# Kernel tuning notes

Measured on AMD Instinct MI355X. Metric: run time of the kernel, lower is better.

The kernel has to match this reference:

```python
import jax, jax.numpy as jnp
import numpy as np

OUT_H, OUT_W = 7, 7
SPATIAL_SCALE = 1.0  # aligned=True (align_corners=True interpolate), per init_kwargs


def setup_inputs() -> dict:
    key = jax.random.key(0)
    kf, kb, kx, ky, kw, kh = jax.random.split(key, 6)
    B, C, H, W = 4, 256, 200, 200
    N = 512
    features = jax.random.normal(kf, (B, C, H, W), dtype=jnp.float32)
    batch_idx = jax.random.randint(kb, (N,), 0, B, dtype=jnp.int32)
    # integer boxes with x2>x1, y2>y1, strictly inside the map
    x1 = jax.random.randint(kx, (N,), 0, W - 64, dtype=jnp.int32)
    y1 = jax.random.randint(ky, (N,), 0, H - 64, dtype=jnp.int32)
    bw = jax.random.randint(kw, (N,), 8, 64, dtype=jnp.int32)
    bh = jax.random.randint(kh, (N,), 8, 64, dtype=jnp.int32)
    x2 = jnp.minimum(x1 + bw, W - 1)
    y2 = jnp.minimum(y1 + bh, H - 1)
    rois = jnp.stack([batch_idx, x1, y1, x2, y2], axis=1)  # [N, 5] int32
    return {"features": features, "rois": rois}


def reference(features, rois):
    # features: [B, C, H, W]; rois: [N, 5] int32 (batch, x1, y1, x2, y2)
    # Faithful to: crop features[b, :, y1:y2+1, x1:x2+1] then
    # F.interpolate(size=(7,7), mode='bilinear', align_corners=True).
    N = rois.shape[0]
    H, W = features.shape[2], features.shape[3]
    b = rois[:, 0]
    coords = rois[:, 1:5].astype(jnp.float32) * SPATIAL_SCALE
    x1, y1, x2, y2 = coords[:, 0], coords[:, 1], coords[:, 2], coords[:, 3]

    # align_corners=True source coords inside the crop, offset into the full map
    jy = jnp.arange(OUT_H, dtype=jnp.float32)
    jx = jnp.arange(OUT_W, dtype=jnp.float32)
    sy = y1[:, None] + jy[None, :] * (y2 - y1)[:, None] / (OUT_H - 1)  # [N, OH]
    sx = x1[:, None] + jx[None, :] * (x2 - x1)[:, None] / (OUT_W - 1)  # [N, OW]

    y0f = jnp.floor(sy); x0f = jnp.floor(sx)
    wy = sy - y0f                                  # [N, OH]
    wx = sx - x0f                                  # [N, OW]
    y0 = jnp.clip(y0f.astype(jnp.int32), 0, H - 1)
    y1i = jnp.clip(y0 + 1, 0, H - 1)
    x0 = jnp.clip(x0f.astype(jnp.int32), 0, W - 1)
    x1i = jnp.clip(x0 + 1, 0, W - 1)

    bb = b[:, None, None]                          # [N,1,1]

    def gather(yi, xi):
        # advanced indexing -> [N, OH, OW, C]
        return features[bb, :, yi[:, :, None], xi[:, None, :]]

    v00 = gather(y0, x0)
    v01 = gather(y0, x1i)
    v10 = gather(y1i, x0)
    v11 = gather(y1i, x1i)

    wyb = wy[:, :, None, None]                     # [N, OH, 1, 1]
    wxb = wx[:, None, :, None]                     # [N, 1, OW, 1]
    out = (v00 * (1 - wyb) * (1 - wxb) + v01 * (1 - wyb) * wxb
           + v10 * wyb * (1 - wxb) + v11 * wyb * wxb)  # [N, OH, OW, C]
    return jnp.transpose(out, (0, 3, 1, 2))        # [N, C, OH, OW]
```

## Files before the change

kernel.cpp:

```cpp
#include <hip/hip_runtime.h>
#include <hip/hip_bf16.h>
#include <string.h>

#define OUT_H 7
#define OUT_W 7
#define FEAT_H 200
#define FEAT_W 200
#define HWB  64
#define LSTR 258

__device__ inline unsigned pack2_bf16(float a, float b) {
    __hip_bfloat16 ha = __float2bfloat16(a);
    __hip_bfloat16 hb = __float2bfloat16(b);
    unsigned short ua, ub;
    memcpy(&ua, &ha, 2);
    memcpy(&ub, &hb, 2);
    return (unsigned)ua | ((unsigned)ub << 16);
}

__global__ __launch_bounds__(256) void nchw_to_nhwc_bf16(
    const float* __restrict__ in,
    __hip_bfloat16* __restrict__ out,
    int HW)
{
    __shared__ float tile[HWB * LSTR];
    int hw0 = blockIdx.x * HWB;
    int b   = blockIdx.y;
    const float* inb = in + (size_t)b * 256 * HW;

    int lane = threadIdx.x & 63;
    int wave = threadIdx.x >> 6;
    int hw   = hw0 + lane;

#pragma unroll 8
    for (int cc = 0; cc < 64; ++cc) {
        int c = (wave << 6) + cc;
        tile[lane * LSTR + c] = inb[(size_t)c * HW + hw];
    }
    __syncthreads();

    unsigned* ob = (unsigned*)(out + ((size_t)b * HW + hw0) * 256);
    int t = threadIdx.x;
#pragma unroll 4
    for (int i = 0; i < 32; ++i) {
        int p   = i * 256 + t;
        int j2  = p * 2;
        int hwr = j2 >> 8;
        int c   = j2 & 255;
        float2 v = *(const float2*)&tile[hwr * LSTR + c];
        ob[p] = pack2_bf16(v.x, v.y);
    }
}

__global__ __launch_bounds__(256) void roialign_nhwc_bf16(
    const __hip_bfloat16* __restrict__ featT,
    const int*   __restrict__ rois,
    float*       __restrict__ out)
{
    __shared__ float acc[256 * OUT_H * OUT_W];
    const int H = FEAT_H, W = FEAT_W;
    int n = blockIdx.x;
    int c = threadIdx.x;

    const int* r = rois + n * 5;
    int   b   = r[0];
    float x1f = (float)r[1];
    float y1f = (float)r[2];
    float dx  = (float)r[3] - x1f;
    float dy  = (float)r[4] - y1f;

    const __hip_bfloat16* fb = featT + (size_t)b * (H * W) * 256 + c;

    for (int jy = 0; jy < OUT_H; ++jy) {
        float sy   = y1f + ((float)jy * dy) / (float)(OUT_H - 1);
        float y0fl = floorf(sy);
        float wy   = sy - y0fl;
        int y0  = min(max((int)y0fl, 0), H - 1);
        int y1i = min(y0 + 1, H - 1);
        float omwy = 1.0f - wy;
        const __hip_bfloat16* row0 = fb + (size_t)(y0  * W) * 256;
        const __hip_bfloat16* row1 = fb + (size_t)(y1i * W) * 256;

#pragma unroll
        for (int jx = 0; jx < OUT_W; ++jx) {
            float sx   = x1f + ((float)jx * dx) / (float)(OUT_W - 1);
            float x0fl = floorf(sx);
            float wx   = sx - x0fl;
            int x0  = min(max((int)x0fl, 0), W - 1);
            int x1i = min(x0 + 1, W - 1);
            float omwx = 1.0f - wx;

            float v00 = __bfloat162float(row0[(size_t)x0  * 256]);
            float v01 = __bfloat162float(row0[(size_t)x1i * 256]);
            float v10 = __bfloat162float(row1[(size_t)x0  * 256]);
            float v11 = __bfloat162float(row1[(size_t)x1i * 256]);

            acc[c * (OUT_H * OUT_W) + jy * OUT_W + jx] =
                v00 * omwy * omwx + v01 * omwy * wx +
                v10 * wy   * omwx + v11 * wy   * wx;
        }
    }
    __syncthreads();

    float* ob = out + (size_t)n * 256 * (OUT_H * OUT_W);
    int total = 256 * OUT_H * OUT_W;
    for (int k = c; k < total; k += blockDim.x)
        ob[k] = acc[k];
}

__global__ __launch_bounds__(256) void roialign_direct(
    const float* __restrict__ feat, const int* __restrict__ rois,
    float* __restrict__ out, int C, int total)
{
    int idx = blockIdx.x * blockDim.x + threadIdx.x;
    if (idx >= total) return;
    const int H = FEAT_H, W = FEAT_W;
    int jx = idx % OUT_W;
    int t  = idx / OUT_W;
    int jy = t % OUT_H;
    t /= OUT_H;
    int c = t % C;
    int n = t / C;
    const int* r = rois + n * 5;
    int b = r[0];
    float x1 = (float)r[1], y1 = (float)r[2];
    float x2 = (float)r[3], y2 = (float)r[4];
    float sy = y1 + ((float)jy * (y2 - y1)) / (float)(OUT_H - 1);
    float sx = x1 + ((float)jx * (x2 - x1)) / (float)(OUT_W - 1);
    float y0f = floorf(sy), x0f = floorf(sx);
    float wy = sy - y0f, wx = sx - x0f;
    int y0  = min(max((int)y0f, 0), H - 1);
    int y1i = min(y0 + 1, H - 1);
    int x0  = min(max((int)x0f, 0), W - 1);
    int x1i = min(x0 + 1, W - 1);
    const float* fp = feat + ((size_t)b * C + c) * (size_t)(H * W);
    float v00 = fp[y0  * W + x0 ];
    float v01 = fp[y0  * W + x1i];
    float v10 = fp[y1i * W + x0 ];
    float v11 = fp[y1i * W + x1i];
    float omwy = 1.0f - wy, omwx = 1.0f - wx;
    out[idx] = v00 * omwy * omwx + v01 * omwy * wx
             + v10 * wy   * omwx + v11 * wy   * wx;
}

extern "C" void kernel_launch(void* const* d_in, const int* in_sizes, int n_in,
                              void* d_out, int out_size, void* d_ws, size_t ws_size,
                              hipStream_t stream)
{
    const float* feat = (const float*)d_in[0];
    const int*   rois = (const int*)d_in[1];
    float*       out  = (float*)d_out;

    int N  = in_sizes[1] / 5;
    int C  = out_size / (N * OUT_H * OUT_W);
    int HW = FEAT_H * FEAT_W;
    int B  = in_sizes[0] / (C * HW);

    size_t need = (size_t)B * HW * C * sizeof(__hip_bfloat16);
    if (C == 256 && (HW % HWB) == 0 && ws_size >= need) {
        __hip_bfloat16* featT = (__hip_bfloat16*)d_ws;
        dim3 tgrid(HW / HWB, B, 1);
        nchw_to_nhwc_bf16<<<tgrid, 256, 0, stream>>>(feat, featT, HW);
        roialign_nhwc_bf16<<<N, 256, 0, stream>>>(featT, rois, out);
    } else {
        int total = out_size;
        roialign_direct<<<(total + 255) / 256, 256, 0, stream>>>(feat, rois, out, C, total);
    }
}
```

Before: 260.8 us.

## Vectorize NHWC bf16 transpose and ROI gather with wider loads

The NCHW-to-NHWC bf16 transpose now reads float4 along HW and writes packed uint2 (four bf16 channels) per thread, using a smaller 32-position tile with a padded stride. The ROI-align kernel has each thread handle four channels via uint2 loads, with four thread groups splitting the 49 output points, and unpacks bf16 with bit shifts. The aim is fewer, wider memory transactions in both the transpose (the dominant full-tensor pass) and the gather. It adds possible LDS bank conflicts from the strided scalar tile writes and the acc stores.

```diff
diff --git a/kernel.cpp b/kernel.cpp
--- a/kernel.cpp
+++ b/kernel.cpp
@@ -6,8 +6,9 @@
 #define OUT_W 7
 #define FEAT_H 200
 #define FEAT_W 200
-#define HWB  64
-#define LSTR 258
+#define HW_ALL (FEAT_H * FEAT_W)
+#define HWB  32
+#define LSTR 260
 
 __device__ inline unsigned pack2_bf16(float a, float b) {
     __hip_bfloat16 ha = __float2bfloat16(a);
@@ -18,50 +19,56 @@
     return (unsigned)ua | ((unsigned)ub << 16);
 }
 
-__global__ __launch_bounds__(256) void nchw_to_nhwc_bf16(
+__global__ __launch_bounds__(256) void nchw_to_nhwc_bf16_v2(
     const float* __restrict__ in,
-    __hip_bfloat16* __restrict__ out,
+    unsigned*    __restrict__ outu,
     int HW)
 {
     __shared__ float tile[HWB * LSTR];
     int hw0 = blockIdx.x * HWB;
     int b   = blockIdx.y;
-    const float* inb = in + (size_t)b * 256 * HW;
+    const float* inb = in + (size_t)b * 256 * HW + hw0;
 
     int lane = threadIdx.x & 63;
-    int wave = threadIdx.x >> 6;
-    int hw   = hw0 + lane;
+    int w    = threadIdx.x >> 6;
+    int cg   = lane >> 3;
+    int xq   = lane & 7;
+    int hwr  = xq << 2;
 
-#pragma unroll 8
-    for (int cc = 0; cc < 64; ++cc) {
-        int c = (wave << 6) + cc;
-        tile[lane * LSTR + c] = inb[(size_t)c * HW + hw];
+#pragma unroll
+    for (int cc = 0; cc < 8; ++cc) {
+        int c = (w << 6) + (cc << 3) + cg;
+        float4 v = *(const float4*)(inb + (size_t)c * HW + hwr);
+        tile[(hwr + 0) * LSTR + c] = v.x;
+        tile[(hwr + 1) * LSTR + c] = v.y;
+        tile[(hwr + 2) * LSTR + c] = v.z;
+        tile[(hwr + 3) * LSTR + c] = v.w;
     }
     __syncthreads();
 
-    unsigned* ob = (unsigned*)(out + ((size_t)b * HW + hw0) * 256);
+    uint2* ob = (uint2*)outu + ((size_t)b * HW + hw0) * 64;
     int t = threadIdx.x;
-#pragma unroll 4
-    for (int i = 0; i < 32; ++i) {
-        int p   = i * 256 + t;
-        int j2  = p * 2;
-        int hwr = j2 >> 8;
-        int c   = j2 & 255;
-        float2 v = *(const float2*)&tile[hwr * LSTR + c];
-        ob[p] = pack2_bf16(v.x, v.y);
+#pragma unroll
+    for (int i = 0; i < 8; ++i) {
+        int q2  = (i << 8) + t;
+        int hr  = q2 >> 6;
+        int c0  = (q2 & 63) << 2;
+        float4 v = *(const float4*)&tile[hr * LSTR + c0];
+        uint2 o;
+        o.x = pack2_bf16(v.x, v.y);
+        o.y = pack2_bf16(v.z, v.w);
+        ob[q2] = o;
     }
 }
 
-__global__ __launch_bounds__(256) void roialign_nhwc_bf16(
-    const __hip_bfloat16* __restrict__ featT,
+__global__ __launch_bounds__(256) void roialign_nhwc_v2(
+    const uint2* __restrict__ featT2,
     const int*   __restrict__ rois,
     float*       __restrict__ out)
 {
     __shared__ float acc[256 * OUT_H * OUT_W];
     const int H = FEAT_H, W = FEAT_W;
     int n = blockIdx.x;
-    int c = threadIdx.x;
-
     const int* r = rois + n * 5;
     int   b   = r[0];
     float x1f = (float)r[1];
@@ -69,42 +76,54 @@
     float dx  = (float)r[3] - x1f;
     float dy  = (float)r[4] - y1f;
 
-    const __hip_bfloat16* fb = featT + (size_t)b * (H * W) * 256 + c;
+    int t  = threadIdx.x;
+    int pg = t >> 6;
+    int cq = t & 63;
+    const uint2* fb = featT2 + (size_t)b * HW_ALL * 64 + cq;
 
-    for (int jy = 0; jy < OUT_H; ++jy) {
-        float sy   = y1f + ((float)jy * dy) / (float)(OUT_H - 1);
-        float y0fl = floorf(sy);
-        float wy   = sy - y0fl;
-        int y0  = min(max((int)y0fl, 0), H - 1);
-        int y1i = min(y0 + 1, H - 1);
-        float omwy = 1.0f - wy;
-        const __hip_bfloat16* row0 = fb + (size_t)(y0  * W) * 256;
-        const __hip_bfloat16* row1 = fb + (size_t)(y1i * W) * 256;
+#define BFLO(u) __uint_as_float((u) << 16)
+#define BFHI(u) __uint_as_float((u) & 0xffff0000u)
 
 #pragma unroll
-        for (int jx = 0; jx < OUT_W; ++jx) {
-            float sx   = x1f + ((float)jx * dx) / (float)(OUT_W - 1);
-            float x0fl = floorf(sx);
-            float wx   = sx - x0fl;
+    for (int pi = 0; pi < 13; ++pi) {
+        int p = (pi << 2) + pg;
+        if (p < 49) {
+            int jy = p / 7, jx = p % 7;
+            float sy = y1f + ((float)jy * dy) / 6.0f;
+            float sx = x1f + ((float)jx * dx) / 6.0f;
+            float y0fl = floorf(sy), x0fl = floorf(sx);
+            float wy = sy - y0fl,    wx = sx - x0fl;
+            int y0  = min(max((int)y0fl, 0), H - 1);
+            int y1i = min(y0 + 1, H - 1);
             int x0  = min(max((int)x0fl, 0), W - 1);
             int x1i = min(x0 + 1, W - 1);
-            float omwx = 1.0f - wx;
+            float omwy = 1.0f - wy, omwx = 1.0f - wx;
+            float w00 = omwy * omwx, w01 = omwy * wx;
+            float w10 = wy * omwx,   w11 = wy * wx;
 
-            float v00 = __bfloat162float(row0[(size_t)x0  * 256]);
-            float v01 = __bfloat162float(row0[(size_t)x1i * 256]);
-            float v10 = __bfloat162float(row1[(size_t)x0  * 256]);
-            float v11 = __bfloat162float(row1[(size_t)x1i * 256]);
+            const uint2* row0 = fb + (size_t)(y0  * W) * 64;
+            const uint2* row1 = fb + (size_t)(y1i * W) * 64;
+            uint2 u00 = row0[(size_t)x0  * 64];
+            uint2 u01 = row0[(size_t)x1i * 64];
+            uint2 u10 = row1[(size_t)x0  * 64];
+            uint2 u11 = row1[(size_t)x1i * 64];
 
-            acc[c * (OUT_H * OUT_W) + jy * OUT_W + jx] =
-                v00 * omwy * omwx + v01 * omwy * wx +
-                v10 * wy   * omwx + v11 * wy   * wx;
+            float r0 = BFLO(u00.x)*w00 + BFLO(u01.x)*w01 + BFLO(u10.x)*w10 + BFLO(u11.x)*w11;
+            float r1 = BFHI(u00.x)*w00 + BFHI(u01.x)*w01 + BFHI(u10.x)*w10 + BFHI(u11.x)*w11;
+            float r2 = BFLO(u00.y)*w00 + BFLO(u01.y)*w01 + BFLO(u10.y)*w10 + BFLO(u11.y)*w11;
+            float r3 = BFHI(u00.y)*w00 + BFHI(u01.y)*w01 + BFHI(u10.y)*w10 + BFHI(u11.y)*w11;
+
+            int c0 = cq << 2;
+            acc[(c0 + 0) * 49 + p] = r0;
+            acc[(c0 + 1) * 49 + p] = r1;
+            acc[(c0 + 2) * 49 + p] = r2;
+            acc[(c0 + 3) * 49 + p] = r3;
         }
     }
     __syncthreads();
 
-    float* ob = out + (size_t)n * 256 * (OUT_H * OUT_W);
-    int total = 256 * OUT_H * OUT_W;
-    for (int k = c; k < total; k += blockDim.x)
+    float* ob = out + (size_t)n * (256 * OUT_H * OUT_W);
+    for (int k = t; k < 256 * OUT_H * OUT_W; k += 256)
         ob[k] = acc[k];
 }
 
@@ -158,10 +177,10 @@
 
     size_t need = (size_t)B * HW * C * sizeof(__hip_bfloat16);
     if (C == 256 && (HW % HWB) == 0 && ws_size >= need) {
-        __hip_bfloat16* featT = (__hip_bfloat16*)d_ws;
+        unsigned* featT = (unsigned*)d_ws;
         dim3 tgrid(HW / HWB, B, 1);
-        nchw_to_nhwc_bf16<<<tgrid, 256, 0, stream>>>(feat, featT, HW);
-        roialign_nhwc_bf16<<<N, 256, 0, stream>>>(featT, rois, out);
+        nchw_to_nhwc_bf16_v2<<<tgrid, 256, 0, stream>>>(feat, featT, HW);
+        roialign_nhwc_v2<<<N, 256, 0, stream>>>((const uint2*)featT, rois, out);
     } else {
         int total = out_size;
         roialign_direct<<<(total + 255) / 256, 256, 0, stream>>>(feat, rois, out, C, total);
```

Result: no change. 259.9 us (-0.3%).
